# Optimization experiments

Measured on AMD Instinct MI355X. Metric: run time of the kernel, lower is better.

Reference implementation:

```python
import jax, jax.numpy as jnp
import numpy as np

N = 4096  # scaled-up NBNEUR


def setup_inputs() -> dict:
    key = jax.random.key(0)
    k1, k2, k3, k4, k5 = jax.random.split(key, 5)
    # small scales keep tanh out of saturation, like the 0.01 init in the source
    return {
        "input": jax.random.normal(k1, (1, N), dtype=jnp.float32) * 0.1,
        "yin": jax.random.normal(k2, (1, N), dtype=jnp.float32) * 0.1,
        "hebb": jax.random.normal(k3, (N, N), dtype=jnp.float32) * 0.01,
        "w": jax.random.normal(k4, (N, N), dtype=jnp.float32) * 0.01,
        "alpha": jax.random.normal(k5, (N, N), dtype=jnp.float32) * 0.01,
        "eta": jnp.full((1,), 0.01, dtype=jnp.float32),
    }


def reference(input, yin, hebb, w, alpha, eta):
    # yout = tanh(yin @ (w + alpha * hebb) + input)   -> [1, N]
    yout = jnp.tanh(yin @ (w + alpha * hebb) + input)
    # hebb' = (1 - eta) * hebb + eta * outer(yin, yout)  -> [N, N]
    outer = yin[0][:, None] * yout[0][None, :]
    hebb_new = (1.0 - eta) * hebb + eta * outer
    return yout, hebb_new
```

## Files before the change

### kernel.cpp

```cpp
#include <hip/hip_runtime.h>

#define NN 4096
#define ROW_BLOCKS 256
#define ROWS_PER_BLOCK (NN / ROW_BLOCKS)

__global__ __launch_bounds__(256) void matvec_partial_kernel(
    const float* __restrict__ yin,
    const float* __restrict__ w,
    const float* __restrict__ alpha,
    const float* __restrict__ hebb,
    float* __restrict__ t_acc)
{
    const int col = blockIdx.x * 1024 + threadIdx.x * 4;
    const int r0  = blockIdx.y * ROWS_PER_BLOCK;

    float4 acc = make_float4(0.f, 0.f, 0.f, 0.f);
    #pragma unroll
    for (int ii = 0; ii < ROWS_PER_BLOCK; ++ii) {
        const int i = r0 + ii;
        const float yv = yin[i];
        const size_t off = (size_t)i * NN + col;
        const float4 wv = *reinterpret_cast<const float4*>(w + off);
        const float4 av = *reinterpret_cast<const float4*>(alpha + off);
        const float4 hv = *reinterpret_cast<const float4*>(hebb + off);
        acc.x += yv * (wv.x + av.x * hv.x);
        acc.y += yv * (wv.y + av.y * hv.y);
        acc.z += yv * (wv.z + av.z * hv.z);
        acc.w += yv * (wv.w + av.w * hv.w);
    }
    atomicAdd(&t_acc[col + 0], acc.x);
    atomicAdd(&t_acc[col + 1], acc.y);
    atomicAdd(&t_acc[col + 2], acc.z);
    atomicAdd(&t_acc[col + 3], acc.w);
}

__global__ __launch_bounds__(256) void yout_kernel(
    const float* __restrict__ t_acc,
    const float* __restrict__ input,
    float* __restrict__ yout)
{
    const int j = blockIdx.x * 256 + threadIdx.x;
    yout[j] = tanhf(t_acc[j] + input[j]);
}

__global__ __launch_bounds__(256) void hebb_update_kernel(
    const float* __restrict__ hebb,
    const float* __restrict__ yin,
    const float* __restrict__ yout,
    const float* __restrict__ eta_p,
    float* __restrict__ hebb_out)
{
    const float eta = eta_p[0];
    const float om  = 1.0f - eta;
    const int total4 = NN * NN / 4;
    const int stride = gridDim.x * blockDim.x;
    for (int g = blockIdx.x * blockDim.x + threadIdx.x; g < total4; g += stride) {
        const int row = g >> 10;
        const float ye = eta * yin[row];
        const float4 h  = reinterpret_cast<const float4*>(hebb)[g];
        const float4 yo = reinterpret_cast<const float4*>(yout)[g & 1023];
        float4 r;
        r.x = om * h.x + ye * yo.x;
        r.y = om * h.y + ye * yo.y;
        r.z = om * h.z + ye * yo.z;
        r.w = om * h.w + ye * yo.w;
        reinterpret_cast<float4*>(hebb_out)[g] = r;
    }
}

extern "C" void kernel_launch(void* const* d_in, const int* in_sizes, int n_in,
                              void* d_out, int out_size, void* d_ws, size_t ws_size,
                              hipStream_t stream) {
    const float* input = (const float*)d_in[0];
    const float* yin   = (const float*)d_in[1];
    const float* hebb  = (const float*)d_in[2];
    const float* w     = (const float*)d_in[3];
    const float* alpha = (const float*)d_in[4];
    const float* eta   = (const float*)d_in[5];

    float* out      = (float*)d_out;
    float* yout     = out;
    float* hebb_out = out + NN;
    float* t_acc    = (float*)d_ws;

    hipMemsetAsync(t_acc, 0, NN * sizeof(float), stream);

    dim3 g1(NN / 1024, ROW_BLOCKS);
    matvec_partial_kernel<<<g1, 256, 0, stream>>>(yin, w, alpha, hebb, t_acc);

    yout_kernel<<<NN / 256, 256, 0, stream>>>(t_acc, input, yout);

    hebb_update_kernel<<<2048, 256, 0, stream>>>(hebb, yin, yout, eta, hebb_out);
}
```

Before: 247.6 us.

## Replace atomic column accumulation with partial-sum buffer and separate reduction

The matvec kernel now writes per-row-block partial sums to a workspace buffer instead of issuing atomicAdds, and a new reduction kernel sums the partials and applies tanh. This drops the memset and the atomic contention on 4096 columns. Both the matvec and the hebb update kernels batch their loads ahead of compute to raise memory-level parallelism. The cost is an extra 4 MB partial buffer that is written and then read back, and the atomic path remains as a fallback when the workspace is too small.

Result: no change. 244.9 us (-1.1%).

```diff
diff --git a/kernel.cpp b/kernel.cpp
--- a/kernel.cpp
+++ b/kernel.cpp
@@ -1,37 +1,76 @@
 #include <hip/hip_runtime.h>
 
 #define NN 4096
-#define ROW_BLOCKS 256
-#define ROWS_PER_BLOCK (NN / ROW_BLOCKS)
+#define CB 4
+#define RPB 16
+#define RBATCH 4
+#define YB (NN / RPB)
 
+template <int PARTIAL>
 __global__ __launch_bounds__(256) void matvec_partial_kernel(
     const float* __restrict__ yin,
     const float* __restrict__ w,
     const float* __restrict__ alpha,
     const float* __restrict__ hebb,
-    float* __restrict__ t_acc)
+    float* __restrict__ part)
 {
     const int col = blockIdx.x * 1024 + threadIdx.x * 4;
-    const int r0  = blockIdx.y * ROWS_PER_BLOCK;
+    const int r0  = blockIdx.y * RPB;
 
     float4 acc = make_float4(0.f, 0.f, 0.f, 0.f);
     #pragma unroll
-    for (int ii = 0; ii < ROWS_PER_BLOCK; ++ii) {
-        const int i = r0 + ii;
-        const float yv = yin[i];
-        const size_t off = (size_t)i * NN + col;
-        const float4 wv = *reinterpret_cast<const float4*>(w + off);
-        const float4 av = *reinterpret_cast<const float4*>(alpha + off);
-        const float4 hv = *reinterpret_cast<const float4*>(hebb + off);
-        acc.x += yv * (wv.x + av.x * hv.x);
-        acc.y += yv * (wv.y + av.y * hv.y);
-        acc.z += yv * (wv.z + av.z * hv.z);
-        acc.w += yv * (wv.w + av.w * hv.w);
+    for (int b = 0; b < RPB / RBATCH; ++b) {
+        float4 wv[RBATCH], av[RBATCH], hv[RBATCH];
+        float  yv[RBATCH];
+        #pragma unroll
+        for (int k = 0; k < RBATCH; ++k) {
+            const int i = r0 + b * RBATCH + k;
+            const size_t off = (size_t)i * NN + col;
+            wv[k] = *reinterpret_cast<const float4*>(w + off);
+            av[k] = *reinterpret_cast<const float4*>(alpha + off);
+            hv[k] = *reinterpret_cast<const float4*>(hebb + off);
+            yv[k] = yin[i];
+        }
+        #pragma unroll
+        for (int k = 0; k < RBATCH; ++k) {
+            acc.x += yv[k] * (wv[k].x + av[k].x * hv[k].x);
+            acc.y += yv[k] * (wv[k].y + av[k].y * hv[k].y);
+            acc.z += yv[k] * (wv[k].z + av[k].z * hv[k].z);
+            acc.w += yv[k] * (wv[k].w + av[k].w * hv[k].w);
+        }
     }
-    atomicAdd(&t_acc[col + 0], acc.x);
-    atomicAdd(&t_acc[col + 1], acc.y);
-    atomicAdd(&t_acc[col + 2], acc.z);
-    atomicAdd(&t_acc[col + 3], acc.w);
+
+    if (PARTIAL) {
+        *reinterpret_cast<float4*>(part + (size_t)blockIdx.y * NN + col) = acc;
+    } else {
+        atomicAdd(&part[col + 0], acc.x);
+        atomicAdd(&part[col + 1], acc.y);
+        atomicAdd(&part[col + 2], acc.z);
+        atomicAdd(&part[col + 3], acc.w);
+    }
+}
+
+__global__ __launch_bounds__(256) void reduce_yout_kernel(
+    const float* __restrict__ part,
+    const float* __restrict__ input,
+    float* __restrict__ yout)
+{
+    const int tid   = threadIdx.x;
+    const int j     = blockIdx.x * 64 + (tid & 63);
+    const int slice = tid >> 6;
+
+    float s = 0.f;
+    #pragma unroll 8
+    for (int kk = 0; kk < YB / 4; ++kk)
+        s += part[(size_t)(slice * (YB / 4) + kk) * NN + j];
+
+    __shared__ float sm[256];
+    sm[tid] = s;
+    __syncthreads();
+    if (tid < 64) {
+        float tot = sm[tid] + sm[tid + 64] + sm[tid + 128] + sm[tid + 192];
+        yout[j] = tanhf(tot + input[j]);
+    }
 }
 
 __global__ __launch_bounds__(256) void yout_kernel(
@@ -52,18 +91,27 @@
 {
     const float eta = eta_p[0];
     const float om  = 1.0f - eta;
-    const int total4 = NN * NN / 4;
-    const int stride = gridDim.x * blockDim.x;
-    for (int g = blockIdx.x * blockDim.x + threadIdx.x; g < total4; g += stride) {
-        const int row = g >> 10;
-        const float ye = eta * yin[row];
-        const float4 h  = reinterpret_cast<const float4*>(hebb)[g];
-        const float4 yo = reinterpret_cast<const float4*>(yout)[g & 1023];
+    const int tid   = blockIdx.x * 256 + threadIdx.x;
+    const int NT    = 2048 * 256;
+
+    const float4 yo = reinterpret_cast<const float4*>(yout)[tid & 1023];
+
+    float4 hv[8];
+    float  ye[8];
+    #pragma unroll
+    for (int it = 0; it < 8; ++it) {
+        const int g = tid + it * NT;
+        hv[it] = reinterpret_cast<const float4*>(hebb)[g];
+        ye[it] = eta * yin[g >> 10];
+    }
+    #pragma unroll
+    for (int it = 0; it < 8; ++it) {
+        const int g = tid + it * NT;
         float4 r;
-        r.x = om * h.x + ye * yo.x;
-        r.y = om * h.y + ye * yo.y;
-        r.z = om * h.z + ye * yo.z;
-        r.w = om * h.w + ye * yo.w;
+        r.x = om * hv[it].x + ye[it] * yo.x;
+        r.y = om * hv[it].y + ye[it] * yo.y;
+        r.z = om * hv[it].z + ye[it] * yo.z;
+        r.w = om * hv[it].w + ye[it] * yo.w;
         reinterpret_cast<float4*>(hebb_out)[g] = r;
     }
 }
@@ -81,14 +129,20 @@
     float* out      = (float*)d_out;
     float* yout     = out;
     float* hebb_out = out + NN;
-    float* t_acc    = (float*)d_ws;
 
-    hipMemsetAsync(t_acc, 0, NN * sizeof(float), stream);
+    const size_t part_bytes = (size_t)YB * NN * sizeof(float);
+    dim3 g1(CB, YB);
 
-    dim3 g1(NN / 1024, ROW_BLOCKS);
-    matvec_partial_kernel<<<g1, 256, 0, stream>>>(yin, w, alpha, hebb, t_acc);
-
-    yout_kernel<<<NN / 256, 256, 0, stream>>>(t_acc, input, yout);
+    if (ws_size >= part_bytes) {
+        float* part = (float*)d_ws;
+        matvec_partial_kernel<1><<<g1, 256, 0, stream>>>(yin, w, alpha, hebb, part);
+        reduce_yout_kernel<<<NN / 64, 256, 0, stream>>>(part, input, yout);
+    } else {
+        float* t_acc = (float*)d_ws;
+        hipMemsetAsync(t_acc, 0, NN * sizeof(float), stream);
+        matvec_partial_kernel<0><<<g1, 256, 0, stream>>>(yin, w, alpha, hebb, t_acc);
+        yout_kernel<<<NN / 256, 256, 0, stream>>>(t_acc, input, yout);
+    }
 
     hebb_update_kernel<<<2048, 256, 0, stream>>>(hebb, yin, yout, eta, hebb_out);
 }
```
